# Kernel tuning notes

Hardware: AMD Instinct MI355X
Metric: run time of the kernel (lower is better)

The kernel has to match this reference:

```python
import jax, jax.numpy as jnp
import numpy as np

D_MODEL = 1024
N_HEADS = 16
DH = D_MODEL // N_HEADS            # 64
Q_PROJ = D_MODEL // 2              # 512
KV_PROJ = 2 * D_MODEL // 3         # 682
LN_EPS = 1e-5                      # torch.nn.LayerNorm default


def _layernorm(x, gamma, beta, eps=LN_EPS):
    mu = jnp.mean(x, axis=-1, keepdims=True)
    var = jnp.mean(jnp.square(x - mu), axis=-1, keepdims=True)
    return (x - mu) * jax.lax.rsqrt(var + eps) * gamma + beta


def setup_inputs() -> dict:
    key = jax.random.key(0)
    ks = jax.random.split(key, 6)
    B, L = 2, 2048
    x = jax.random.normal(ks[0], (B, L, D_MODEL), dtype=jnp.float32)
    W_dq = 0.01 * jax.random.normal(ks[1], (D_MODEL, Q_PROJ), dtype=jnp.float32)
    W_uq = 0.01 * jax.random.normal(ks[2], (Q_PROJ, D_MODEL), dtype=jnp.float32)
    W_dkv = 0.01 * jax.random.normal(ks[3], (D_MODEL, KV_PROJ), dtype=jnp.float32)
    W_ukv = 0.01 * jax.random.normal(ks[4], (KV_PROJ, 2 * D_MODEL), dtype=jnp.float32)
    q_gamma = jnp.ones((Q_PROJ,), jnp.float32)
    q_beta = jnp.zeros((Q_PROJ,), jnp.float32)
    kv_gamma = jnp.ones((KV_PROJ,), jnp.float32)
    kv_beta = jnp.zeros((KV_PROJ,), jnp.float32)
    return {"x": x, "W_dq": W_dq, "W_uq": W_uq, "q_gamma": q_gamma,
            "q_beta": q_beta, "W_dkv": W_dkv, "W_ukv": W_ukv,
            "kv_gamma": kv_gamma, "kv_beta": kv_beta}


def reference(x, W_dq, W_uq, q_gamma, q_beta, W_dkv, W_ukv, kv_gamma, kv_beta):
    B, L, _ = x.shape
    # low-rank Q path: down-project, layernorm, up-project
    compressed_q = _layernorm(x @ W_dq, q_gamma, q_beta)      # [B,L,Q_PROJ]
    Q = compressed_q @ W_uq                                    # [B,L,D]
    # low-rank joint KV path
    compressed_kv = _layernorm(x @ W_dkv, kv_gamma, kv_beta)  # [B,L,KV_PROJ]
    KV = compressed_kv @ W_ukv                                 # [B,L,2D]
    K, V = KV[..., :D_MODEL], KV[..., D_MODEL:]
    # split heads: [B,H,L,dh]
    q = Q.reshape(B, L, N_HEADS, DH).transpose(0, 2, 1, 3)
    k = K.reshape(B, L, N_HEADS, DH).transpose(0, 2, 1, 3)
    v = V.reshape(B, L, N_HEADS, DH).transpose(0, 2, 1, 3)
    scores = jnp.einsum('bhqd,bhkd->bhqk', q, k) / jnp.sqrt(jnp.float32(DH))
    attn = jax.nn.softmax(scores, axis=-1)                     # [B,H,L,L]
    # NOTE: original forward computes feat = LN(dropout(fc(attn@v)) + x) but
    # discards it, returning (x, attn, compressed_kv). Dead code omitted.
    return (x, attn, compressed_kv)
```

## Files before the change

kernel.cpp:

```cpp
#include <hip/hip_runtime.h>

typedef __bf16 bf16;
typedef __bf16 bf16x4 __attribute__((ext_vector_type(4)));
typedef __bf16 bf16x8 __attribute__((ext_vector_type(8)));
typedef float f32x4 __attribute__((ext_vector_type(4)));

#define GCAST(p) ((const __attribute__((address_space(1))) void*)(p))
#define LCAST(p) ((__attribute__((address_space(3))) void*)(p))

#define ML 4096
#define DM 1024
#define QP 512
#define KVP 682
#define KVPP 768
#define NDOWN 1280

__device__ __forceinline__ void trans_tile(const float* __restrict__ src, int srcLD,
                                           int K, int N, int NP,
                                           bf16* __restrict__ dst, int dstLD, int dn,
                                           int bx, int by, float (*tile)[65]) {
    const int k0 = bx * 64, n0 = by * 64;
    const int c = threadIdx.x & 63, r4 = threadIdx.x >> 6;
    #pragma unroll
    for (int rr = r4; rr < 64; rr += 4) {
        int k = k0 + rr, n = n0 + c;
        tile[rr][c] = (k < K && n < N) ? src[(size_t)k * srcLD + n] : 0.f;
    }
    __syncthreads();
    #pragma unroll
    for (int nn = r4; nn < 64; nn += 4) {
        int n = n0 + nn, k = k0 + c;
        if (n < NP && k < dstLD)
            dst[(size_t)(n + dn) * dstLD + k] = (bf16)tile[c][nn];
    }
}

__global__ __launch_bounds__(256) void prep(const f32x4* __restrict__ x4,
                                            f32x4* __restrict__ out0,
                                            bf16* __restrict__ xb,
                                            const float* __restrict__ Wdq,
                                            const float* __restrict__ Wdkv,
                                            const float* __restrict__ Wuq,
                                            const float* __restrict__ Wukv,
                                            bf16* __restrict__ Wdt,
                                            bf16* __restrict__ Wuqt,
                                            bf16* __restrict__ Wukvt) {
    __shared__ float tile[64][65];
    int bid = blockIdx.x;
    if (bid < 4096) {
        int i = bid * 256 + threadIdx.x;
        f32x4 v = x4[i];
        __builtin_nontemporal_store(v, &out0[i]);
        bf16x4 b;
        b[0] = (bf16)v.x; b[1] = (bf16)v.y; b[2] = (bf16)v.z; b[3] = (bf16)v.w;
        *(bf16x4*)(xb + (size_t)i * 4) = b;
        return;
    }
    int rel = bid - 4096;
    if (rel < 128) {
        trans_tile(Wdq, QP, DM, QP, QP, Wdt, DM, 0, rel & 15, rel >> 4, tile);
    } else if (rel < 320) {
        rel -= 128;
        trans_tile(Wdkv, KVP, DM, KVP, KVPP, Wdt, DM, QP, rel & 15, rel >> 4, tile);
    } else if (rel < 448) {
        rel -= 320;
        trans_tile(Wuq, DM, QP, DM, DM, Wuqt, QP, 0, rel & 7, rel >> 3, tile);
    } else {
        rel -= 448;
        trans_tile(Wukv, 2048, KVP, DM, DM, Wukvt, KVPP, 0, rel % 12, rel / 12, tile);
    }
}

__device__ __forceinline__ void gemm_body(const bf16* __restrict__ A,
                                          const bf16* __restrict__ Bt,
                                          bf16* __restrict__ C,
                                          int N, int K, int bx, int by,
                                          bf16* As, bf16* Bs) {
    const int t = threadIdx.x;
    const int w = t >> 6, lane = t & 63;
    const int bm = bx * 128, bn = by * 128;
    const int wr = (w >> 1) * 64, wc = (w & 1) * 64;
    const int r16 = lane & 15, g4 = lane >> 4;
    const int srow = w * 16 + (lane >> 2);
    const int scol = (lane & 3) * 8;

    f32x4 acc[4][4] = {};

    for (int k0 = 0; k0 < K; k0 += 32) {
        #pragma unroll
        for (int r = 0; r < 2; ++r) {
            const bf16* ga = A + (size_t)(bm + r*64 + srow) * K + k0 + scol;
            __builtin_amdgcn_global_load_lds(GCAST(ga), LCAST(&As[r*2048 + w*512]), 16, 0, 0);
            const bf16* gb = Bt + (size_t)(bn + r*64 + srow) * K + k0 + scol;
            __builtin_amdgcn_global_load_lds(GCAST(gb), LCAST(&Bs[r*2048 + w*512]), 16, 0, 0);
        }
        __syncthreads();
        bf16x8 af[4], bfr[4];
        #pragma unroll
        for (int i = 0; i < 4; ++i)
            af[i] = *(const bf16x8*)&As[(wr + i*16 + r16) * 32 + g4*8];
        #pragma unroll
        for (int j = 0; j < 4; ++j)
            bfr[j] = *(const bf16x8*)&Bs[(wc + j*16 + r16) * 32 + g4*8];
        #pragma unroll
        for (int i = 0; i < 4; ++i)
            #pragma unroll
            for (int j = 0; j < 4; ++j)
                acc[i][j] = __builtin_amdgcn_mfma_f32_16x16x32_bf16(af[i], bfr[j], acc[i][j], 0, 0, 0);
        __syncthreads();
    }
    #pragma unroll
    for (int i = 0; i < 4; ++i)
        #pragma unroll
        for (int j = 0; j < 4; ++j)
            #pragma unroll
            for (int r = 0; r < 4; ++r) {
                int row = bm + wr + i*16 + g4*4 + r;
                int col = bn + wc + j*16 + r16;
                C[(size_t)row * N + col] = (bf16)acc[i][j][r];
            }
}

__global__ __launch_bounds__(256) void gemm_down(const bf16* __restrict__ A,
                                                 const bf16* __restrict__ Bt,
                                                 bf16* __restrict__ C) {
    __shared__ bf16 As[128 * 32];
    __shared__ bf16 Bs[128 * 32];
    gemm_body(A, Bt, C, NDOWN, DM, blockIdx.x, blockIdx.y, As, Bs);
}

__global__ __launch_bounds__(256) void gemm_up2(const bf16* __restrict__ Cq,
                                                const bf16* __restrict__ Wuqt,
                                                bf16* __restrict__ Qb,
                                                const bf16* __restrict__ Ckv,
                                                const bf16* __restrict__ Wukvt,
                                                bf16* __restrict__ Kb) {
    __shared__ bf16 As[128 * 32];
    __shared__ bf16 Bs[128 * 32];
    if (blockIdx.z == 0)
        gemm_body(Cq,  Wuqt,  Qb, DM, QP,   blockIdx.x, blockIdx.y, As, Bs);
    else
        gemm_body(Ckv, Wukvt, Kb, DM, KVPP, blockIdx.x, blockIdx.y, As, Bs);
}

__device__ __forceinline__ void block_reduce2(float& s, float& sq) {
    #pragma unroll
    for (int m = 1; m < 64; m <<= 1) {
        s  += __shfl_xor(s, m);
        sq += __shfl_xor(sq, m);
    }
    __shared__ float ls[4], lq[4];
    int w = threadIdx.x >> 6;
    __syncthreads();
    if ((threadIdx.x & 63) == 0) { ls[w] = s; lq[w] = sq; }
    __syncthreads();
    s  = ls[0] + ls[1] + ls[2] + ls[3];
    sq = lq[0] + lq[1] + lq[2] + lq[3];
}

__global__ __launch_bounds__(256) void ln_fused(const bf16* __restrict__ Cdown,
                                                const float* __restrict__ qg,
                                                const float* __restrict__ qb,
                                                const float* __restrict__ kvg,
                                                const float* __restrict__ kvb,
                                                bf16* __restrict__ Cq,
                                                float* __restrict__ out2,
                                                bf16* __restrict__ Ckv) {
    const int row = blockIdx.x, t = threadIdx.x;
    const bf16* src = Cdown + (size_t)row * NDOWN;

    {
        float v0 = (float)src[t], v1 = (float)src[t + 256];
        float s = v0 + v1, sq = v0*v0 + v1*v1;
        block_reduce2(s, sq);
        float mu = s * (1.f/512.f);
        float var = sq * (1.f/512.f) - mu*mu;
        float rs = rsqrtf(var + 1e-5f);
        Cq[(size_t)row*QP + t]       = (bf16)((v0 - mu)*rs*qg[t]     + qb[t]);
        Cq[(size_t)row*QP + t + 256] = (bf16)((v1 - mu)*rs*qg[t+256] + qb[t+256]);
    }
    {
        const bf16* skv = src + QP;
        float v[3];
        float s = 0.f, sq = 0.f;
        #pragma unroll
        for (int i = 0; i < 3; ++i) {
            int j = t + i*256;
            v[i] = (j < KVP) ? (float)skv[j] : 0.f;
            s += v[i]; sq += v[i]*v[i];
        }
        block_reduce2(s, sq);
        float mu = s * (1.f/682.f);
        float var = sq * (1.f/682.f) - mu*mu;
        float rs = rsqrtf(var + 1e-5f);
        #pragma unroll
        for (int i = 0; i < 3; ++i) {
            int j = t + i*256;
            if (j < KVP) {
                float y = (v[i]-mu)*rs*kvg[j] + kvb[j];
                __builtin_nontemporal_store(y, &out2[(size_t)row*KVP + j]);
                Ckv[(size_t)row*KVPP + j] = (bf16)y;
            } else if (j < KVPP) {
                Ckv[(size_t)row*KVPP + j] = (bf16)0.f;
            }
        }
    }
}

__global__ __launch_bounds__(512, 2) void attn_k(const bf16* __restrict__ Qb,
                                                 const bf16* __restrict__ Kb,
                                                 float* __restrict__ out1) {
    const int t = threadIdx.x, w = t >> 6, lane = t & 63;
    const int flat = blockIdx.x;
    const int xcd = flat & 7, local = flat >> 3;
    const int qblk = local & 127;
    const int bh = (xcd << 2) | (local >> 7);
    const int b = bh >> 4, h = bh & 15;
    const int q0 = qblk * 16;
    __shared__ bf16 Qs[16 * 64];
    __shared__ float reds[8][16];

    for (int i = t; i < 1024; i += 512) {
        int qr = i >> 6, d = i & 63;
        Qs[i] = Qb[(size_t)(b*2048 + q0 + qr) * DM + h*64 + d];
    }
    __syncthreads();

    const int r16 = lane & 15, g4 = lane >> 4;
    bf16x8 a0 = *(const bf16x8*)&Qs[r16*64 + g4*8];
    bf16x8 a1 = *(const bf16x8*)&Qs[r16*64 + 32 + g4*8];

    const bf16* kbase = Kb + (size_t)b * 2048 * DM + h*64;
    const int colw = w * 256;

    f32x4 acc[16];
    #pragma unroll
    for (int ni = 0; ni < 16; ++ni) {
        const bf16* kr = kbase + (size_t)(colw + ni*16 + r16) * DM + g4*8;
        bf16x8 b0 = *(const bf16x8*)kr;
        bf16x8 b1 = *(const bf16x8*)(kr + 32);
        f32x4 c = {};
        c = __builtin_amdgcn_mfma_f32_16x16x32_bf16(a0, b0, c, 0, 0, 0);
        c = __builtin_amdgcn_mfma_f32_16x16x32_bf16(a1, b1, c, 0, 0, 0);
        acc[ni] = c;
    }

    float sm[4] = {0.f, 0.f, 0.f, 0.f};
    #pragma unroll
    for (int ni = 0; ni < 16; ++ni)
        #pragma unroll
        for (int r = 0; r < 4; ++r) {
            float e = __expf(acc[ni][r] * 0.125f);
            acc[ni][r] = e;
            sm[r] += e;
        }
    #pragma unroll
    for (int m = 1; m < 16; m <<= 1)
        #pragma unroll
        for (int r = 0; r < 4; ++r) sm[r] += __shfl_xor(sm[r], m);
    if (r16 == 0) {
        #pragma unroll
        for (int r = 0; r < 4; ++r) reds[w][g4*4 + r] = sm[r];
    }
    __syncthreads();
    float inv[4];
    #pragma unroll
    for (int r = 0; r < 4; ++r) {
        int row = g4*4 + r;
        float s = 0.f;
        #pragma unroll
        for (int ww = 0; ww < 8; ++ww) s += reds[ww][row];
        inv[r] = 1.f / s;
    }

    float* obase = out1 + ((size_t)bh * 2048 + q0) * 2048 + colw;
    #pragma unroll
    for (int ni = 0; ni < 16; ++ni)
        #pragma unroll
        for (int r = 0; r < 4; ++r)
            obase[(size_t)(g4*4 + r) * 2048 + ni*16 + r16] = acc[ni][r] * inv[r];
}

extern "C" void kernel_launch(void* const* d_in, const int* in_sizes, int n_in,
                              void* d_out, int out_size, void* d_ws, size_t ws_size,
                              hipStream_t stream) {
    const float* x    = (const float*)d_in[0];
    const float* Wdq  = (const float*)d_in[1];
    const float* Wuq  = (const float*)d_in[2];
    const float* qg   = (const float*)d_in[3];
    const float* qbt  = (const float*)d_in[4];
    const float* Wdkv = (const float*)d_in[5];
    const float* Wukv = (const float*)d_in[6];
    const float* kvg  = (const float*)d_in[7];
    const float* kvb  = (const float*)d_in[8];

    float* out0 = (float*)d_out;
    float* out1 = out0 + (size_t)4194304;
    float* out2 = out1 + (size_t)134217728;

    char* ws = (char*)d_ws;
    bf16* Xbf   = (bf16*)(ws + 0);
    bf16* Wdt   = (bf16*)(ws + 8388608);
    bf16* Wuqt  = (bf16*)(ws + 11010048);
    bf16* Wukvt = (bf16*)(ws + 12058624);
    bf16* Cdown = (bf16*)(ws + 13631488);
    bf16* Cq    = (bf16*)(ws + 24117248);
    bf16* Ckv   = (bf16*)(ws + 28311552);
    bf16* Qb    = (bf16*)(ws + 34603008);
    bf16* Kb    = (bf16*)(ws + 42991616);

    prep<<<4736, 256, 0, stream>>>((const f32x4*)x, (f32x4*)out0, Xbf,
                                   Wdq, Wdkv, Wuq, Wukv, Wdt, Wuqt, Wukvt);
    gemm_down<<<dim3(ML/128, NDOWN/128), 256, 0, stream>>>(Xbf, Wdt, Cdown);
    ln_fused<<<ML, 256, 0, stream>>>(Cdown, qg, qbt, kvg, kvb, Cq, out2, Ckv);
    gemm_up2<<<dim3(ML/128, DM/128, 2), 256, 0, stream>>>(Cq, Wuqt, Qb, Ckv, Wukvt, Kb);
    attn_k<<<4096, 512, 0, stream>>>(Qb, Kb, out1);
}
```

Measured before the change: 249.2 us.

## Transpose MFMA operands so softmax rows sit per lane, vectorize nontemporal stores

Swaps the A/B operands of the score MFMA so each lane holds four consecutive key columns of a single query row instead of four rows. This replaces the 4-way, 16-lane shuffle reduction with two cross-group shuffles of one scalar. It also lets the attention output be written as 16-byte vector stores with nontemporal hints instead of scattered scalar stores. The large attention matrix write is the dominant cost, so wider, streaming stores aim to improve write bandwidth.

```diff
diff --git a/kernel.cpp b/kernel.cpp
--- a/kernel.cpp
+++ b/kernel.cpp
@@ -227,8 +227,8 @@
     __syncthreads();
 
     const int r16 = lane & 15, g4 = lane >> 4;
-    bf16x8 a0 = *(const bf16x8*)&Qs[r16*64 + g4*8];
-    bf16x8 a1 = *(const bf16x8*)&Qs[r16*64 + 32 + g4*8];
+    bf16x8 qf0 = *(const bf16x8*)&Qs[r16*64 + g4*8];
+    bf16x8 qf1 = *(const bf16x8*)&Qs[r16*64 + 32 + g4*8];
 
     const bf16* kbase = Kb + (size_t)b * 2048 * DM + h*64;
     const int colw = w * 256;
@@ -237,48 +237,38 @@
     #pragma unroll
     for (int ni = 0; ni < 16; ++ni) {
         const bf16* kr = kbase + (size_t)(colw + ni*16 + r16) * DM + g4*8;
-        bf16x8 b0 = *(const bf16x8*)kr;
-        bf16x8 b1 = *(const bf16x8*)(kr + 32);
+        bf16x8 k0 = *(const bf16x8*)kr;
+        bf16x8 k1 = *(const bf16x8*)(kr + 32);
         f32x4 c = {};
-        c = __builtin_amdgcn_mfma_f32_16x16x32_bf16(a0, b0, c, 0, 0, 0);
-        c = __builtin_amdgcn_mfma_f32_16x16x32_bf16(a1, b1, c, 0, 0, 0);
+        c = __builtin_amdgcn_mfma_f32_16x16x32_bf16(k0, qf0, c, 0, 0, 0);
+        c = __builtin_amdgcn_mfma_f32_16x16x32_bf16(k1, qf1, c, 0, 0, 0);
         acc[ni] = c;
     }
 
-    float sm[4] = {0.f, 0.f, 0.f, 0.f};
+    float sm = 0.f;
     #pragma unroll
     for (int ni = 0; ni < 16; ++ni)
         #pragma unroll
         for (int r = 0; r < 4; ++r) {
             float e = __expf(acc[ni][r] * 0.125f);
             acc[ni][r] = e;
-            sm[r] += e;
+            sm += e;
         }
-    #pragma unroll
-    for (int m = 1; m < 16; m <<= 1)
-        #pragma unroll
-        for (int r = 0; r < 4; ++r) sm[r] += __shfl_xor(sm[r], m);
-    if (r16 == 0) {
-        #pragma unroll
-        for (int r = 0; r < 4; ++r) reds[w][g4*4 + r] = sm[r];
-    }
-    __syncthreads();
-    float inv[4];
-    #pragma unroll
-    for (int r = 0; r < 4; ++r) {
-        int row = g4*4 + r;
-        float s = 0.f;
-        #pragma unroll
-        for (int ww = 0; ww < 8; ++ww) s += reds[ww][row];
-        inv[r] = 1.f / s;
-    }
-
-    float* obase = out1 + ((size_t)bh * 2048 + q0) * 2048 + colw;
-    #pragma unroll
-    for (int ni = 0; ni < 16; ++ni)
-        #pragma unroll
-        for (int r = 0; r < 4; ++r)
-            obase[(size_t)(g4*4 + r) * 2048 + ni*16 + r16] = acc[ni][r] * inv[r];
+    sm += __shfl_xor(sm, 16);
+    sm += __shfl_xor(sm, 32);
+    if (g4 == 0) reds[w][r16] = sm;
+    __syncthreads();
+    float s = 0.f;
+    #pragma unroll
+    for (int ww = 0; ww < 8; ++ww) s += reds[ww][r16];
+    float inv = 1.f / s;
+
+    float* obase = out1 + ((size_t)(bh * 2048 + q0 + r16)) * 2048 + colw + g4*4;
+    #pragma unroll
+    for (int ni = 0; ni < 16; ++ni) {
+        f32x4 v = acc[ni] * inv;
+        __builtin_nontemporal_store(v, (f32x4*)(obase + ni*16));
+    }
 }
 
 extern "C" void kernel_launch(void* const* d_in, const int* in_sizes, int n_in,
```

Result: slower. 254.9 us (+2.3%).
